# Kernel tuning notes

Hardware: AMD Instinct MI355X
Metric: run time of the kernel (lower is better)

The kernel has to match this reference:

```python
import jax, jax.numpy as jnp
import numpy as np

N_NODES = 100000
N_EDGES = 1600000
DROPOUT_P = 0.5


def setup_inputs() -> dict:
    key = jax.random.key(0)
    k1, k2, k3, k4 = jax.random.split(key, 4)
    x = jax.random.normal(k1, (N_NODES, 128), dtype=jnp.float32)
    edge_index = jax.random.randint(k2, (2, N_EDGES), 0, N_NODES, dtype=jnp.int64)
    W1 = jax.random.normal(k3, (128, 64), dtype=jnp.float32) * (1.0 / np.sqrt(128))
    b1 = jnp.zeros((64,), dtype=jnp.float32)
    W2 = jax.random.normal(k4, (64, 40), dtype=jnp.float32) * (1.0 / np.sqrt(64))
    b2 = jnp.zeros((40,), dtype=jnp.float32)
    return {"x": x, "edge_index": edge_index, "W1": W1, "b1": b1, "W2": W2, "b2": b2}


def reference(x, edge_index, W1, b1, W2, b2):
    n = x.shape[0]
    src, dst = edge_index[0], edge_index[1]
    # GCN symmetric normalization with self-loops: deg = A.sum + 1
    deg = jax.ops.segment_sum(jnp.ones(src.shape[0], x.dtype), dst, num_segments=n) + 1.0
    inv_sqrt = jax.lax.rsqrt(deg)  # [N]
    edge_norm = (inv_sqrt[src] * inv_sqrt[dst])[:, None]  # [E,1]
    self_norm = (inv_sqrt * inv_sqrt)[:, None]            # [N,1]

    def propagate(h):
        # gather source features, scale, scatter-add to destinations; add self-loop term
        agg = jax.ops.segment_sum(h[src] * edge_norm, dst, num_segments=n)
        return agg + h * self_norm

    # layer 1: linear -> aggregate -> bias -> relu -> dropout
    h = propagate(x @ W1) + b1
    h = jax.nn.relu(h)
    keep = 1.0 - DROPOUT_P
    mask = jax.random.bernoulli(jax.random.key(42), keep, h.shape)
    h = jnp.where(mask, h / keep, 0.0)
    # layer 2
    out = propagate(h @ W2) + b2
    return out
```

## Files before the change

kernel.cpp:

```cpp
#include <hip/hip_runtime.h>

#define NN 100000
#define NE 1600000
#define FI 128
#define FH 64
#define FO 40
#define NR 500
#define RSZ 200
#define NBK 512

typedef _Float16 f16;
typedef _Float16 f16x2 __attribute__((ext_vector_type(2)));

__device__ __forceinline__ unsigned rotl32(unsigned v, unsigned r) {
    return (v << r) | (v >> (32u - r));
}

__device__ __forceinline__ void threefry_0_42(unsigned x0, unsigned x1,
                                              unsigned& o0, unsigned& o1) {
    const unsigned k0 = 0u, k1 = 42u;
    const unsigned k2 = 0x1BD11BDAu ^ k0 ^ k1;
    x0 += k0; x1 += k1;
#define TFR(r) { x0 += x1; x1 = rotl32(x1, r); x1 ^= x0; }
    TFR(13) TFR(15) TFR(26) TFR(6)   x0 += k1; x1 += k2 + 1u;
    TFR(17) TFR(29) TFR(16) TFR(24)  x0 += k2; x1 += k0 + 2u;
    TFR(13) TFR(15) TFR(26) TFR(6)   x0 += k0; x1 += k1 + 3u;
    TFR(17) TFR(29) TFR(16) TFR(24)  x0 += k1; x1 += k2 + 4u;
    TFR(13) TFR(15) TFR(26) TFR(6)   x0 += k2; x1 += k0 + 5u;
#undef TFR
    o0 = x0; o1 = x1;
}

__device__ __forceinline__ void unpack2(unsigned u, float& lo, float& hi) {
    union { unsigned u; f16 h[2]; } c;
    c.u = u;
    lo = (float)c.h[0];
    hi = (float)c.h[1];
}

__device__ __forceinline__ int sel4(int p, int s0, int s1, int s2, int s3) {
    int t0 = (p & 1) ? s1 : s0;
    int t1 = (p & 1) ? s3 : s2;
    return (p & 2) ? t1 : t0;
}

__global__ __launch_bounds__(256) void k_p1(const int* __restrict__ ei,
                                            int* __restrict__ blkhist) {
    __shared__ int h[NR];
    int t = threadIdx.x, b = blockIdx.x;
    for (int i = t; i < NR; i += 256) h[i] = 0;
    __syncthreads();
    for (int base = b * 512 + t * 2; base < NE; base += NBK * 512) {
        int2 dd = *(const int2*)&ei[NE + base];
        atomicAdd(&h[dd.x / RSZ], 1);
        atomicAdd(&h[dd.y / RSZ], 1);
    }
    __syncthreads();
    for (int i = t; i < NR; i += 256) blkhist[(size_t)b * NR + i] = h[i];
}

__global__ __launch_bounds__(512) void k_scanR1(int* __restrict__ blkhist,
                                                int* __restrict__ rtot) {
    __shared__ int sh[NBK];
    int r = blockIdx.x, t = threadIdx.x;
    int v = blkhist[(size_t)t * NR + r];
    sh[t] = v;
    __syncthreads();
    for (int off = 1; off < NBK; off <<= 1) {
        int u = (t >= off) ? sh[t - off] : 0;
        __syncthreads();
        sh[t] += u;
        __syncthreads();
    }
    blkhist[(size_t)t * NR + r] = sh[t] - v;
    if (t == NBK - 1) rtot[r] = sh[t];
}

__global__ __launch_bounds__(512) void k_scanR2(const int* __restrict__ rtot,
                                                int* __restrict__ rangeBase) {
    __shared__ int sh[512];
    int t = threadIdx.x;
    int v = (t < NR) ? rtot[t] : 0;
    sh[t] = v;
    __syncthreads();
    for (int off = 1; off < 512; off <<= 1) {
        int u = (t >= off) ? sh[t - off] : 0;
        __syncthreads();
        sh[t] += u;
        __syncthreads();
    }
    if (t < NR) rangeBase[t] = sh[t] - v;
    if (t == NR - 1) rangeBase[NR] = sh[t];
}

__global__ __launch_bounds__(256) void k_p2(const int* __restrict__ ei,
                                            const int* __restrict__ blkhist,
                                            const int* __restrict__ rangeBase,
                                            int* __restrict__ bucket) {
    __shared__ int cur[NR];
    int t = threadIdx.x, b = blockIdx.x;
    for (int i = t; i < NR; i += 256)
        cur[i] = rangeBase[i] + blkhist[(size_t)b * NR + i];
    __syncthreads();
    for (int base = b * 512 + t * 2; base < NE; base += NBK * 512) {
        int2 ss = *(const int2*)&ei[base];
        int2 dd = *(const int2*)&ei[NE + base];
        int rg0 = dd.x / RSZ;
        int rg1 = dd.y / RSZ;
        int pos0 = atomicAdd(&cur[rg0], 1);
        bucket[pos0] = ((dd.x - rg0 * RSZ) << 17) | ss.x;
        int pos1 = atomicAdd(&cur[rg1], 1);
        bucket[pos1] = ((dd.y - rg1 * RSZ) << 17) | ss.y;
    }
}

__global__ __launch_bounds__(256) void k_p3(const int* __restrict__ bucket,
                                            const int* __restrict__ rangeBase,
                                            int2* __restrict__ odpk,
                                            float* __restrict__ inv,
                                            int* __restrict__ csr_s) {
    __shared__ int cnt[RSZ];
    __shared__ int base[RSZ];
    __shared__ int sc[256];
    int r = blockIdx.x, t = threadIdx.x;
    int e0 = rangeBase[r], e1 = rangeBase[r + 1];
    int padBase = e0 + 3 * RSZ * r;
    int n0 = r * RSZ;
    if (t < RSZ) cnt[t] = 0;
    __syncthreads();
    for (int i = e0 + t; i < e1; i += 256)
        atomicAdd(&cnt[((unsigned)bucket[i]) >> 17], 1);
    __syncthreads();
    int v = 0, vp = 0;
    if (t < RSZ) {
        v = cnt[t];
        vp = (v + 3) & ~3;
    }
    sc[t] = vp;
    __syncthreads();
    for (int off = 1; off < 256; off <<= 1) {
        int u = (t >= off) ? sc[t - off] : 0;
        __syncthreads();
        sc[t] += u;
        __syncthreads();
    }
    int o = 0;
    if (t < RSZ) {
        o = padBase + sc[t] - vp;
        odpk[n0 + t] = make_int2(o, vp);
        inv[n0 + t] = rsqrtf((float)v + 1.0f);
        base[t] = o;
    }
    __syncthreads();
    for (int i = e0 + t; i < e1; i += 256) {
        int pk = bucket[i];
        int dloc = ((unsigned)pk) >> 17;
        int p = atomicAdd(&base[dloc], 1);
        csr_s[p] = pk & 0x1FFFF;
    }
    __syncthreads();
    if (t < RSZ) {
        for (int j = v; j < vp; ++j) csr_s[o + j] = NN;
    }
}

#define XS_STRIDE 68
__global__ __launch_bounds__(256) void k_gemm1(const float* __restrict__ x,
                                               const float* __restrict__ W1,
                                               const float* __restrict__ inv,
                                               f16* __restrict__ h0s) {
    __shared__ float xs[64 * XS_STRIDE];
    __shared__ float ws[64 * FH];
    int t = threadIdx.x;
    int row0 = blockIdx.x * 64;
    float acc[4][4] = {{0.f}};
    int tx4 = (t & 15) * 4;
    int ty4 = (t >> 4) * 4;
    int sr = t >> 4;
    int sc4 = (t & 15) * 4;
#pragma unroll
    for (int half = 0; half < 2; ++half) {
        __syncthreads();
#pragma unroll
        for (int p = 0; p < 4; ++p) {
            int row = row0 + sr + p * 16;
            float4 v = make_float4(0.f, 0.f, 0.f, 0.f);
            if (row < NN) v = *(const float4*)&x[(size_t)row * FI + half * 64 + sc4];
            *(float4*)&xs[(sr + p * 16) * XS_STRIDE + sc4] = v;
        }
        {
            const float4* Wv = (const float4*)(W1 + half * 64 * FH);
            float4* wv = (float4*)ws;
            for (int i = t; i < 64 * FH / 4; i += 256) wv[i] = Wv[i];
        }
        __syncthreads();
#pragma unroll 2
        for (int k = 0; k < 64; k += 4) {
            float4 a0 = *(const float4*)&xs[(ty4 + 0) * XS_STRIDE + k];
            float4 a1 = *(const float4*)&xs[(ty4 + 1) * XS_STRIDE + k];
            float4 a2 = *(const float4*)&xs[(ty4 + 2) * XS_STRIDE + k];
            float4 a3 = *(const float4*)&xs[(ty4 + 3) * XS_STRIDE + k];
            float4 b0 = *(const float4*)&ws[(k + 0) * FH + tx4];
            float4 b1 = *(const float4*)&ws[(k + 1) * FH + tx4];
            float4 b2 = *(const float4*)&ws[(k + 2) * FH + tx4];
            float4 b3 = *(const float4*)&ws[(k + 3) * FH + tx4];
#define KK1(AE, BV) \
            acc[0][0] = fmaf(a0.AE, BV.x, acc[0][0]); \
            acc[0][1] = fmaf(a0.AE, BV.y, acc[0][1]); \
            acc[0][2] = fmaf(a0.AE, BV.z, acc[0][2]); \
            acc[0][3] = fmaf(a0.AE, BV.w, acc[0][3]); \
            acc[1][0] = fmaf(a1.AE, BV.x, acc[1][0]); \
            acc[1][1] = fmaf(a1.AE, BV.y, acc[1][1]); \
            acc[1][2] = fmaf(a1.AE, BV.z, acc[1][2]); \
            acc[1][3] = fmaf(a1.AE, BV.w, acc[1][3]); \
            acc[2][0] = fmaf(a2.AE, BV.x, acc[2][0]); \
            acc[2][1] = fmaf(a2.AE, BV.y, acc[2][1]); \
            acc[2][2] = fmaf(a2.AE, BV.z, acc[2][2]); \
            acc[2][3] = fmaf(a2.AE, BV.w, acc[2][3]); \
            acc[3][0] = fmaf(a3.AE, BV.x, acc[3][0]); \
            acc[3][1] = fmaf(a3.AE, BV.y, acc[3][1]); \
            acc[3][2] = fmaf(a3.AE, BV.z, acc[3][2]); \
            acc[3][3] = fmaf(a3.AE, BV.w, acc[3][3]);
            KK1(x, b0) KK1(y, b1) KK1(z, b2) KK1(w, b3)
#undef KK1
        }
    }
#pragma unroll
    for (int i = 0; i < 4; ++i) {
        int row = row0 + ty4 + i;
        if (row < NN) {
            float s = inv[row];
            union { f16 h[4]; uint2 u; } p;
            p.h[0] = (f16)(acc[i][0] * s);
            p.h[1] = (f16)(acc[i][1] * s);
            p.h[2] = (f16)(acc[i][2] * s);
            p.h[3] = (f16)(acc[i][3] * s);
            *(uint2*)&h0s[(size_t)row * FH + tx4] = p.u;
        } else if (row == NN) {
            *(uint2*)&h0s[(size_t)row * FH + tx4] = make_uint2(0u, 0u);
        }
    }
}

__global__ __launch_bounds__(256) void k_agg1(const int2* __restrict__ odpk,
                                              const int* __restrict__ csr_s,
                                              const float* __restrict__ inv,
                                              const f16* __restrict__ h0s,
                                              const float* __restrict__ b1,
                                              f16* __restrict__ h1s) {
    int lane = threadIdx.x & 63;
    int d = __builtin_amdgcn_readfirstlane((int)(blockIdx.x * 4 + (threadIdx.x >> 6)));
    if (d >= NN) return;
    int p = lane >> 4;
    int c4 = (lane & 15) * 4;
    size_t q8 = (size_t)(lane & 15) * 8;
    const char* hb = (const char*)h0s;
    int2 od = odpk[d];
    int start = od.x, degp = od.y;
    float a0 = 0.f, a1 = 0.f, a2 = 0.f, a3 = 0.f;
    int k = 0;
    for (; k + 8 <= degp; k += 8) {
        int s0 = csr_s[start + k + 0], s1 = csr_s[start + k + 1];
        int s2 = csr_s[start + k + 2], s3 = csr_s[start + k + 3];
        int s4 = csr_s[start + k + 4], s5 = csr_s[start + k + 5];
        int s6 = csr_s[start + k + 6], s7 = csr_s[start + k + 7];
        int ia = sel4(p, s0, s1, s2, s3);
        int ib = sel4(p, s4, s5, s6, s7);
        union { uint2 u; f16x2 h[2]; } A, B;
        A.u = *(const uint2*)(hb + ((size_t)ia << 7) + q8);
        B.u = *(const uint2*)(hb + ((size_t)ib << 7) + q8);
        f16x2 p0 = A.h[0] + B.h[0];
        f16x2 p1 = A.h[1] + B.h[1];
        a0 += (float)p0[0]; a1 += (float)p0[1];
        a2 += (float)p1[0]; a3 += (float)p1[1];
    }
    if (k < degp) {
        int s0 = csr_s[start + k + 0], s1 = csr_s[start + k + 1];
        int s2 = csr_s[start + k + 2], s3 = csr_s[start + k + 3];
        int ia = sel4(p, s0, s1, s2, s3);
        uint2 ua = *(const uint2*)(hb + ((size_t)ia << 7) + q8);
        float f0, f1, f2, f3;
        unpack2(ua.x, f0, f1); unpack2(ua.y, f2, f3);
        a0 += f0; a1 += f1; a2 += f2; a3 += f3;
    }
    a0 += __shfl_xor(a0, 16, 64); a0 += __shfl_xor(a0, 32, 64);
    a1 += __shfl_xor(a1, 16, 64); a1 += __shfl_xor(a1, 32, 64);
    a2 += __shfl_xor(a2, 16, 64); a2 += __shfl_xor(a2, 32, 64);
    a3 += __shfl_xor(a3, 16, 64); a3 += __shfl_xor(a3, 32, 64);
    float invd = inv[d];
    uint2 su = *(const uint2*)(hb + ((size_t)d << 7) + q8);
    float s0, s1, s2, s3;
    unpack2(su.x, s0, s1); unpack2(su.y, s2, s3);
    float4 bv = *(const float4*)&b1[c4];
    float v0 = fmaxf((a0 + s0) * invd + bv.x, 0.f);
    float v1 = fmaxf((a1 + s1) * invd + bv.y, 0.f);
    float v2 = fmaxf((a2 + s2) * invd + bv.z, 0.f);
    float v3 = fmaxf((a3 + s3) * invd + bv.w, 0.f);
    unsigned o0, o1;
    threefry_0_42(0u, (unsigned)(d * FH + lane), o0, o1);
    unsigned long long m = __ballot((int)(((o0 ^ o1) >> 31) ^ 1u));
    unsigned mm = (unsigned)(m >> c4) & 15u;
    if (lane < 16) {
        union { f16 h[4]; uint2 u; } st;
        st.h[0] = (f16)((mm & 1u) ? v0 * 2.f : 0.f);
        st.h[1] = (f16)((mm & 2u) ? v1 * 2.f : 0.f);
        st.h[2] = (f16)((mm & 4u) ? v2 * 2.f : 0.f);
        st.h[3] = (f16)((mm & 8u) ? v3 * 2.f : 0.f);
        *(uint2*)&h1s[(size_t)d * FH + c4] = st.u;
    }
}

#define HS_STRIDE 68
__global__ __launch_bounds__(256) void k_gemm2(const f16* __restrict__ h1s,
                                               const float* __restrict__ W2,
                                               const float* __restrict__ inv,
                                               f16* __restrict__ h2s) {
    __shared__ float hs[64 * HS_STRIDE];
    __shared__ float ws[FH * 64];
    int t = threadIdx.x;
    int row0 = blockIdx.x * 64;
    {
        int r = t >> 4;
        int c4 = (t & 15) * 4;
#pragma unroll
        for (int p = 0; p < 4; ++p) {
            int row = row0 + r + p * 16;
            float4 v = make_float4(0.f, 0.f, 0.f, 0.f);
            if (row < NN) {
                uint2 u = *(const uint2*)&h1s[(size_t)row * FH + c4];
                unpack2(u.x, v.x, v.y);
                unpack2(u.y, v.z, v.w);
            }
            *(float4*)&hs[(r + p * 16) * HS_STRIDE + c4] = v;
        }
    }
    for (int i = t; i < FH * 64; i += 256) {
        int r = i >> 6, c = i & 63;
        ws[i] = (c < FO) ? W2[r * FO + c] : 0.f;
    }
    __syncthreads();
    float acc[4][4] = {{0.f}};
    int tx4 = (t & 15) * 4;
    int ty4 = (t >> 4) * 4;
#pragma unroll 2
    for (int k = 0; k < FH; k += 4) {
        float4 a0 = *(const float4*)&hs[(ty4 + 0) * HS_STRIDE + k];
        float4 a1 = *(const float4*)&hs[(ty4 + 1) * HS_STRIDE + k];
        float4 a2 = *(const float4*)&hs[(ty4 + 2) * HS_STRIDE + k];
        float4 a3 = *(const float4*)&hs[(ty4 + 3) * HS_STRIDE + k];
        float4 b0 = *(const float4*)&ws[(k + 0) * 64 + tx4];
        float4 b1 = *(const float4*)&ws[(k + 1) * 64 + tx4];
        float4 b2 = *(const float4*)&ws[(k + 2) * 64 + tx4];
        float4 b3 = *(const float4*)&ws[(k + 3) * 64 + tx4];
#define KK2(AE, BV) \
        acc[0][0] = fmaf(a0.AE, BV.x, acc[0][0]); \
        acc[0][1] = fmaf(a0.AE, BV.y, acc[0][1]); \
        acc[0][2] = fmaf(a0.AE, BV.z, acc[0][2]); \
        acc[0][3] = fmaf(a0.AE, BV.w, acc[0][3]); \
        acc[1][0] = fmaf(a1.AE, BV.x, acc[1][0]); \
        acc[1][1] = fmaf(a1.AE, BV.y, acc[1][1]); \
        acc[1][2] = fmaf(a1.AE, BV.z, acc[1][2]); \
        acc[1][3] = fmaf(a1.AE, BV.w, acc[1][3]); \
        acc[2][0] = fmaf(a2.AE, BV.x, acc[2][0]); \
        acc[2][1] = fmaf(a2.AE, BV.y, acc[2][1]); \
        acc[2][2] = fmaf(a2.AE, BV.z, acc[2][2]); \
        acc[2][3] = fmaf(a2.AE, BV.w, acc[2][3]); \
        acc[3][0] = fmaf(a3.AE, BV.x, acc[3][0]); \
        acc[3][1] = fmaf(a3.AE, BV.y, acc[3][1]); \
        acc[3][2] = fmaf(a3.AE, BV.z, acc[3][2]); \
        acc[3][3] = fmaf(a3.AE, BV.w, acc[3][3]);
        KK2(x, b0) KK2(y, b1) KK2(z, b2) KK2(w, b3)
#undef KK2
    }
#pragma unroll
    for (int i = 0; i < 4; ++i) {
        int row = row0 + ty4 + i;
        if (row < NN) {
            float s = inv[row];
            union { f16 h[4]; uint2 u; } p;
            p.h[0] = (f16)(acc[i][0] * s);
            p.h[1] = (f16)(acc[i][1] * s);
            p.h[2] = (f16)(acc[i][2] * s);
            p.h[3] = (f16)(acc[i][3] * s);
            *(uint2*)&h2s[(size_t)row * FH + tx4] = p.u;
        } else if (row == NN) {
            *(uint2*)&h2s[(size_t)row * FH + tx4] = make_uint2(0u, 0u);
        }
    }
}

__global__ __launch_bounds__(256) void k_agg2(const int2* __restrict__ odpk,
                                              const int* __restrict__ csr_s,
                                              const float* __restrict__ inv,
                                              const f16* __restrict__ h2s,
                                              const float* __restrict__ b2,
                                              float* __restrict__ out) {
    int lane = threadIdx.x & 63;
    int d = __builtin_amdgcn_readfirstlane((int)(blockIdx.x * 4 + (threadIdx.x >> 6)));
    if (d >= NN) return;
    int p = lane >> 4;
    int c4 = (lane & 15) * 4;
    size_t q8 = (size_t)(lane & 15) * 8;
    const char* hb = (const char*)h2s;
    int2 od = odpk[d];
    int start = od.x, degp = od.y;
    float a0 = 0.f, a1 = 0.f, a2 = 0.f, a3 = 0.f;
    int k = 0;
    for (; k + 8 <= degp; k += 8) {
        int s0 = csr_s[start + k + 0], s1 = csr_s[start + k + 1];
        int s2 = csr_s[start + k + 2], s3 = csr_s[start + k + 3];
        int s4 = csr_s[start + k + 4], s5 = csr_s[start + k + 5];
        int s6 = csr_s[start + k + 6], s7 = csr_s[start + k + 7];
        int ia = sel4(p, s0, s1, s2, s3);
        int ib = sel4(p, s4, s5, s6, s7);
        union { uint2 u; f16x2 h[2]; } A, B;
        A.u = *(const uint2*)(hb + ((size_t)ia << 7) + q8);
        B.u = *(const uint2*)(hb + ((size_t)ib << 7) + q8);
        f16x2 p0 = A.h[0] + B.h[0];
        f16x2 p1 = A.h[1] + B.h[1];
        a0 += (float)p0[0]; a1 += (float)p0[1];
        a2 += (float)p1[0]; a3 += (float)p1[1];
    }
    if (k < degp) {
        int s0 = csr_s[start + k + 0], s1 = csr_s[start + k + 1];
        int s2 = csr_s[start + k + 2], s3 = csr_s[start + k + 3];
        int ia = sel4(p, s0, s1, s2, s3);
        uint2 ua = *(const uint2*)(hb + ((size_t)ia << 7) + q8);
        float f0, f1, f2, f3;
        unpack2(ua.x, f0, f1); unpack2(ua.y, f2, f3);
        a0 += f0; a1 += f1; a2 += f2; a3 += f3;
    }
    a0 += __shfl_xor(a0, 16, 64); a0 += __shfl_xor(a0, 32, 64);
    a1 += __shfl_xor(a1, 16, 64); a1 += __shfl_xor(a1, 32, 64);
    a2 += __shfl_xor(a2, 16, 64); a2 += __shfl_xor(a2, 32, 64);
    a3 += __shfl_xor(a3, 16, 64); a3 += __shfl_xor(a3, 32, 64);
    if (lane < 10) {
        float invd = inv[d];
        uint2 su = *(const uint2*)(hb + ((size_t)d << 7) + q8);
        float s0, s1, s2, s3;
        unpack2(su.x, s0, s1); unpack2(su.y, s2, s3);
        float4 bv = *(const float4*)&b2[c4];
        float4 st;
        st.x = (a0 + s0) * invd + bv.x;
        st.y = (a1 + s1) * invd + bv.y;
        st.z = (a2 + s2) * invd + bv.z;
        st.w = (a3 + s3) * invd + bv.w;
        *(float4*)&out[(size_t)d * FO + c4] = st;
    }
}

extern "C" void kernel_launch(void* const* d_in, const int* in_sizes, int n_in,
                              void* d_out, int out_size, void* d_ws, size_t ws_size,
                              hipStream_t stream) {
    const float* x  = (const float*)d_in[0];
    const int*   ei = (const int*)d_in[1];
    const float* W1 = (const float*)d_in[2];
    const float* b1 = (const float*)d_in[3];
    const float* W2 = (const float*)d_in[4];
    const float* b2 = (const float*)d_in[5];
    float* out = (float*)d_out;

    char* ws = (char*)d_ws;
    int*   blkhist   = (int*)ws;
    int*   rtot      = (int*)(ws + (size_t)(1 << 20) + 102400);
    int*   rangeBase = (int*)(ws + (size_t)(1 << 20) + 106496);
    float* inv       = (float*)(ws + (size_t)( 2 << 20));
    int2*  odpk      = (int2*)(ws + (size_t)( 3 << 20));
    int*   bucket    = (int*)(ws + (size_t)( 4 << 20));
    f16*   h2s       = (f16*)(ws + (size_t)( 4 << 20));
    int*   csr_s     = (int*)(ws + (size_t)(17 << 20));
    f16*   h0s       = (f16*)(ws + (size_t)(25 << 20));
    f16*   h1s       = (f16*)(ws + (size_t)(38 << 20));

    k_p1<<<NBK, 256, 0, stream>>>(ei, blkhist);
    k_scanR1<<<NR, 512, 0, stream>>>(blkhist, rtot);
    k_scanR2<<<1, 512, 0, stream>>>(rtot, rangeBase);
    k_p2<<<NBK, 256, 0, stream>>>(ei, blkhist, rangeBase, bucket);
    k_p3<<<NR, 256, 0, stream>>>(bucket, rangeBase, odpk, inv, csr_s);

    int gblk = (NN + 63) / 64;
    k_gemm1<<<gblk, 256, 0, stream>>>(x, W1, inv, h0s);
    k_agg1<<<NN / 4, 256, 0, stream>>>(odpk, csr_s, inv, h0s, b1, h1s);

    k_gemm2<<<gblk, 256, 0, stream>>>(h1s, W2, inv, h2s);
    k_agg2<<<NN / 4, 256, 0, stream>>>(odpk, csr_s, inv, h2s, b2, out);
}
```

Before: 177.8 us.

## Precompute dropout mask in separate kernel and reduce partial sums in packed f16

Dropout bits are now produced by a standalone threefry kernel that writes one 64-bit ballot mask per node, and the aggregation kernel only loads that mask. The aim is to take the threefry ALU work off the gather-bound critical path. The cross-lane reduction of the four accumulators now runs as packed f16x2 shuffles, halving the shuffle count. The cost is an extra launch with a 0.8 MB mask write and read, plus lower precision in the final reduction, since partial sums are rounded to f16 before adding.

```diff
diff --git a/kernel.cpp b/kernel.cpp
--- a/kernel.cpp
+++ b/kernel.cpp
@@ -42,6 +42,24 @@
     int t0 = (p & 1) ? s1 : s0;
     int t1 = (p & 1) ? s3 : s2;
     return (p & 2) ? t1 : t0;
+}
+
+__device__ __forceinline__ void combine4_f16(float& x, float& y) {
+    union { unsigned u; f16x2 h; } A, B;
+    A.h[0] = (f16)x; A.h[1] = (f16)y;
+    B.u = __shfl_xor(A.u, 16, 64);
+    A.h = A.h + B.h;
+    B.u = __shfl_xor(A.u, 32, 64);
+    A.h = A.h + B.h;
+    x = (float)A.h[0]; y = (float)A.h[1];
+}
+
+__global__ __launch_bounds__(256) void k_mask(unsigned long long* __restrict__ dm) {
+    int tid = blockIdx.x * 256 + threadIdx.x;
+    unsigned o0, o1;
+    threefry_0_42(0u, (unsigned)tid, o0, o1);
+    unsigned long long m = __ballot((int)(((o0 ^ o1) >> 31) ^ 1u));
+    if ((threadIdx.x & 63) == 0) dm[tid >> 6] = m;
 }
 
 __global__ __launch_bounds__(256) void k_p1(const int* __restrict__ ei,
@@ -247,6 +265,7 @@
                                               const float* __restrict__ inv,
                                               const f16* __restrict__ h0s,
                                               const float* __restrict__ b1,
+                                              const unsigned long long* __restrict__ dm,
                                               f16* __restrict__ h1s) {
     int lane = threadIdx.x & 63;
     int d = __builtin_amdgcn_readfirstlane((int)(blockIdx.x * 4 + (threadIdx.x >> 6)));
@@ -283,10 +302,8 @@
         unpack2(ua.x, f0, f1); unpack2(ua.y, f2, f3);
         a0 += f0; a1 += f1; a2 += f2; a3 += f3;
     }
-    a0 += __shfl_xor(a0, 16, 64); a0 += __shfl_xor(a0, 32, 64);
-    a1 += __shfl_xor(a1, 16, 64); a1 += __shfl_xor(a1, 32, 64);
-    a2 += __shfl_xor(a2, 16, 64); a2 += __shfl_xor(a2, 32, 64);
-    a3 += __shfl_xor(a3, 16, 64); a3 += __shfl_xor(a3, 32, 64);
+    combine4_f16(a0, a1);
+    combine4_f16(a2, a3);
     float invd = inv[d];
     uint2 su = *(const uint2*)(hb + ((size_t)d << 7) + q8);
     float s0, s1, s2, s3;
@@ -296,9 +313,7 @@
     float v1 = fmaxf((a1 + s1) * invd + bv.y, 0.f);
     float v2 = fmaxf((a2 + s2) * invd + bv.z, 0.f);
     float v3 = fmaxf((a3 + s3) * invd + bv.w, 0.f);
-    unsigned o0, o1;
-    threefry_0_42(0u, (unsigned)(d * FH + lane), o0, o1);
-    unsigned long long m = __ballot((int)(((o0 ^ o1) >> 31) ^ 1u));
+    unsigned long long m = dm[d];
     unsigned mm = (unsigned)(m >> c4) & 15u;
     if (lane < 16) {
         union { f16 h[4]; uint2 u; } st;
@@ -430,10 +445,8 @@
         unpack2(ua.x, f0, f1); unpack2(ua.y, f2, f3);
         a0 += f0; a1 += f1; a2 += f2; a3 += f3;
     }
-    a0 += __shfl_xor(a0, 16, 64); a0 += __shfl_xor(a0, 32, 64);
-    a1 += __shfl_xor(a1, 16, 64); a1 += __shfl_xor(a1, 32, 64);
-    a2 += __shfl_xor(a2, 16, 64); a2 += __shfl_xor(a2, 32, 64);
-    a3 += __shfl_xor(a3, 16, 64); a3 += __shfl_xor(a3, 32, 64);
+    combine4_f16(a0, a1);
+    combine4_f16(a2, a3);
     if (lane < 10) {
         float invd = inv[d];
         uint2 su = *(const uint2*)(hb + ((size_t)d << 7) + q8);
@@ -471,7 +484,9 @@
     int*   csr_s     = (int*)(ws + (size_t)(17 << 20));
     f16*   h0s       = (f16*)(ws + (size_t)(25 << 20));
     f16*   h1s       = (f16*)(ws + (size_t)(38 << 20));
-
+    unsigned long long* dm = (unsigned long long*)(ws + (size_t)(51 << 20));
+
+    k_mask<<<NN * FH / 256, 256, 0, stream>>>(dm);
     k_p1<<<NBK, 256, 0, stream>>>(ei, blkhist);
     k_scanR1<<<NR, 512, 0, stream>>>(blkhist, rtot);
     k_scanR2<<<1, 512, 0, stream>>>(rtot, rangeBase);
@@ -480,7 +495,7 @@
 
     int gblk = (NN + 63) / 64;
     k_gemm1<<<gblk, 256, 0, stream>>>(x, W1, inv, h0s);
-    k_agg1<<<NN / 4, 256, 0, stream>>>(odpk, csr_s, inv, h0s, b1, h1s);
+    k_agg1<<<NN / 4, 256, 0, stream>>>(odpk, csr_s, inv, h0s, b1, dm, h1s);
 
     k_gemm2<<<gblk, 256, 0, stream>>>(h1s, W2, inv, h2s);
     k_agg2<<<NN / 4, 256, 0, stream>>>(odpk, csr_s, inv, h2s, b2, out);
```

Result: slower. 185.7 us (+4.5%).
